# Kernel tuning notes

Hardware: AMD Instinct MI355X
Metric: run time of the kernel (lower is better)

## Reference

```python
import jax, jax.numpy as jnp
import numpy as np


def setup_inputs() -> dict:
    key = jax.random.key(0)
    B, N, D = 8, 2048, 512
    put = jax.random.normal(key, (B, N, D), dtype=jnp.float32)
    return {"put": put, "k": 16}


def reference(put, k):
    # put: [B, N, D]; k: python int
    B, N, _ = put.shape
    # squared-norm expansion of pairwise Euclidean distance
    xx = jnp.sum(put * put, axis=2, keepdims=True)            # [B, N, 1]
    gram = jnp.einsum('bnd,bmd->bnm', put, put)               # [B, N, N]
    dist2 = xx + jnp.swapaxes(xx, 1, 2) - 2.0 * gram          # [B, N, N]
    dist = jnp.sqrt(jnp.clip(dist2, 0.0))                     # clamp(min=0).sqrt()

    # k nearest (smallest distance): top_k of negated distances
    _, inc = jax.lax.top_k(-dist, k)                          # [B, N, k] int32

    # binary adjacency: out[b, j, inc[b, j, :]] = 1 (vectorized scatter)
    b_idx = jnp.arange(B)[:, None, None]                      # [B,1,1]
    r_idx = jnp.arange(N)[None, :, None]                      # [1,N,1]
    out = jnp.zeros_like(dist).at[b_idx, r_idx, inc].set(1.0)
    return out
```

## Files before the change

### kernel.cpp

```cpp
#include <hip/hip_runtime.h>
#include <cstdint>

#define NN 2048
#define DD 512
#define NB 8
#define NCAND 24

using ull = unsigned long long;
typedef __attribute__((ext_vector_type(8))) short bf16x8;
typedef __attribute__((ext_vector_type(4))) float f32x4;

#define GLOAD_LDS16(g, l)                                                      \
  __builtin_amdgcn_global_load_lds(                                            \
      (const __attribute__((address_space(1))) unsigned int*)(g),              \
      (__attribute__((address_space(3))) unsigned int*)(l), 16, 0, 0)

__device__ inline unsigned short f2bf(float f) {
  unsigned u = __float_as_uint(f);
  unsigned r = u + 0x7FFFu + ((u >> 16) & 1u);
  return (unsigned short)(r >> 16);
}

__global__ __launch_bounds__(256) void knn_prep(const float* __restrict__ put,
                                                float* __restrict__ norms32,
                                                unsigned short* __restrict__ bhalf) {
  const int row  = blockIdx.x * 4 + (threadIdx.x >> 6);
  const int lane = threadIdx.x & 63;
  const float* p = put + (size_t)row * DD + lane * 8;
  float4 x0 = ((const float4*)p)[0];
  float4 x1 = ((const float4*)p)[1];
  double s = (double)x0.x * (double)x0.x + (double)x0.y * (double)x0.y +
             (double)x0.z * (double)x0.z + (double)x0.w * (double)x0.w +
             (double)x1.x * (double)x1.x + (double)x1.y * (double)x1.y +
             (double)x1.z * (double)x1.z + (double)x1.w * (double)x1.w;
  uint4 v;
  v.x = (unsigned)f2bf(x0.x) | ((unsigned)f2bf(x0.y) << 16);
  v.y = (unsigned)f2bf(x0.z) | ((unsigned)f2bf(x0.w) << 16);
  v.z = (unsigned)f2bf(x1.x) | ((unsigned)f2bf(x1.y) << 16);
  v.w = (unsigned)f2bf(x1.z) | ((unsigned)f2bf(x1.w) << 16);
  *((uint4*)(bhalf + (size_t)row * DD) + lane) = v;
#pragma unroll
  for (int m = 1; m < 64; m <<= 1) s += __shfl_xor(s, m, 64);
  if (lane == 0) norms32[row] = (float)s;
}

__global__ __launch_bounds__(256) void knn_gemm(
    const unsigned short* __restrict__ bhalf,
    const float* __restrict__ norms32,
    unsigned short* __restrict__ Sws) {
  __shared__ unsigned short smem[18432];
  unsigned short* As = smem;
  unsigned short* Bs = smem + 4096;

  int idx = blockIdx.x;
  int jt = 0;
  while (idx >= 16 - jt) { idx -= 16 - jt; ++jt; }
  const int mt = jt + idx;

  const int t    = threadIdx.x;
  const int lane = t & 63;
  const int wv   = t >> 6;
  const int q    = lane >> 4;
  const int l15  = lane & 15;
  const int wrow = wv >> 1, wcol = wv & 1;
  const int m0 = mt * 128;
  const int j0 = jt * 128;
  const int b  = blockIdx.y;

  const unsigned short* pb = bhalf + (size_t)b * NN * DD;

  const int rloc = lane >> 2;
  const int kcg  = (lane & 3) ^ ((lane >> 3) & 3);
  const int i0 = 2 * wv, i1 = 2 * wv + 1;
  const unsigned short* gA0 = pb + (size_t)(j0 + 16 * i0 + rloc) * DD + kcg * 8;
  const unsigned short* gA1 = pb + (size_t)(j0 + 16 * i1 + rloc) * DD + kcg * 8;
  const unsigned short* gB0 = pb + (size_t)(m0 + 16 * i0 + rloc) * DD + kcg * 8;
  const unsigned short* gB1 = pb + (size_t)(m0 + 16 * i1 + rloc) * DD + kcg * 8;
  unsigned short* lA0 = As + i0 * 512;
  unsigned short* lA1 = As + i1 * 512;
  unsigned short* lB0 = Bs + i0 * 512;
  unsigned short* lB1 = Bs + i1 * 512;

  const int xsw = (q ^ ((l15 >> 1) & 3)) * 8;

  f32x4 acc[4][4];
  const f32x4 zz = {0.f, 0.f, 0.f, 0.f};
#pragma unroll
  for (int i = 0; i < 4; ++i)
#pragma unroll
    for (int j = 0; j < 4; ++j) acc[i][j] = zz;

  for (int kt = 0; kt < DD; kt += 32) {
    __syncthreads();
    GLOAD_LDS16(gA0, lA0);
    GLOAD_LDS16(gA1, lA1);
    GLOAD_LDS16(gB0, lB0);
    GLOAD_LDS16(gB1, lB1);
    gA0 += 32; gA1 += 32; gB0 += 32; gB1 += 32;
    __syncthreads();

    bf16x8 af[4], bg[4];
#pragma unroll
    for (int f = 0; f < 4; ++f) {
      af[f] = *(const bf16x8*)(As + (wrow * 64 + f * 16 + l15) * 32 + xsw);
      bg[f] = *(const bf16x8*)(Bs + (wcol * 64 + f * 16 + l15) * 32 + xsw);
    }
#pragma unroll
    for (int fi = 0; fi < 4; ++fi)
#pragma unroll
      for (int fj = 0; fj < 4; ++fj)
        acc[fi][fj] = __builtin_amdgcn_mfma_f32_16x16x32_bf16(
            af[fi], bg[fj], acc[fi][fj], 0, 0, 0);
  }

  float xn[4];
#pragma unroll
  for (int fj = 0; fj < 4; ++fj)
    xn[fj] = norms32[(size_t)b * NN + m0 + wcol * 64 + fj * 16 + l15];

  __syncthreads();
  unsigned short* Sl = smem + wv * 4096;
#pragma unroll
  for (int fi = 0; fi < 4; ++fi)
#pragma unroll
    for (int fj = 0; fj < 4; ++fj)
#pragma unroll
      for (int r = 0; r < 4; ++r) {
        float sv = xn[fj] - 2.0f * acc[fi][fj][r] + 2048.0f;
        Sl[(fi * 16 + q * 4 + r) * 64 + fj * 16 + l15] =
            __builtin_bit_cast(unsigned short, (_Float16)sv);
      }

  const size_t row0 = (size_t)(b * NN + j0 + wrow * 64);
#pragma unroll
  for (int it = 0; it < 8; ++it) {
    int i2 = it * 64 + lane;
    int row = i2 >> 3, c8 = i2 & 7;
    uint4 v = *(const uint4*)(Sl + row * 64 + c8 * 8);
    *(uint4*)(Sws + (row0 + row) * NN + m0 + wcol * 64 + c8 * 8) = v;
  }

  if (jt != mt) {
    float xr[16];
#pragma unroll
    for (int fi = 0; fi < 4; ++fi)
#pragma unroll
      for (int r = 0; r < 4; ++r)
        xr[fi * 4 + r] =
            norms32[(size_t)b * NN + j0 + wrow * 64 + fi * 16 + q * 4 + r];

    __syncthreads();
    unsigned short* Mw = smem + wv * 4608;
#pragma unroll
    for (int fi = 0; fi < 4; ++fi)
#pragma unroll
      for (int fj = 0; fj < 4; ++fj)
#pragma unroll
        for (int r = 0; r < 4; ++r) {
          float sv = xr[fi * 4 + r] - 2.0f * acc[fi][fj][r] + 2048.0f;
          Mw[(fj * 16 + l15) * 72 + fi * 16 + q * 4 + r] =
              __builtin_bit_cast(unsigned short, (_Float16)sv);
        }
    const size_t mrow0 = (size_t)(b * NN + m0 + wcol * 64);
#pragma unroll
    for (int it = 0; it < 8; ++it) {
      int i2 = it * 64 + lane;
      int row = i2 >> 3, c8 = i2 & 7;
      uint4 v = *(const uint4*)(Mw + row * 72 + c8 * 8);
      *(uint4*)(Sws + (mrow0 + row) * NN + j0 + wrow * 64 + c8 * 8) = v;
    }
  }
}

#define CEX(a, i, j)                                                           \
  {                                                                            \
    unsigned lo_ = min(a[i], a[j]), hi_ = max(a[i], a[j]);                     \
    a[i] = lo_;                                                                \
    a[j] = hi_;                                                                \
  }

__device__ inline void mk8(unsigned (&a)[8], uint4 u, unsigned base) {
  a[0] = (u.x << 16) | base;
  a[1] = (u.x & 0xFFFF0000u) | (base + 1);
  a[2] = (u.y << 16) | (base + 2);
  a[3] = (u.y & 0xFFFF0000u) | (base + 3);
  a[4] = (u.z << 16) | (base + 4);
  a[5] = (u.z & 0xFFFF0000u) | (base + 5);
  a[6] = (u.w << 16) | (base + 6);
  a[7] = (u.w & 0xFFFF0000u) | (base + 7);
}

__device__ inline void sort8(unsigned (&a)[8]) {
  CEX(a, 0, 1) CEX(a, 2, 3) CEX(a, 4, 5) CEX(a, 6, 7)
  CEX(a, 0, 2) CEX(a, 1, 3) CEX(a, 4, 6) CEX(a, 5, 7)
  CEX(a, 1, 2) CEX(a, 5, 6)
  CEX(a, 0, 4) CEX(a, 1, 5) CEX(a, 2, 6) CEX(a, 3, 7)
  CEX(a, 2, 4) CEX(a, 3, 5)
  CEX(a, 1, 2) CEX(a, 3, 4) CEX(a, 5, 6)
}

__device__ inline void merge8(unsigned (&a)[8], const unsigned (&b)[8]) {
  unsigned t[8];
#pragma unroll
  for (int i = 0; i < 8; ++i) t[i] = min(a[i], b[7 - i]);
  CEX(t, 0, 4) CEX(t, 1, 5) CEX(t, 2, 6) CEX(t, 3, 7)
  CEX(t, 0, 2) CEX(t, 1, 3) CEX(t, 4, 6) CEX(t, 5, 7)
  CEX(t, 0, 1) CEX(t, 2, 3) CEX(t, 4, 5) CEX(t, 6, 7)
#pragma unroll
  for (int i = 0; i < 8; ++i) a[i] = t[i];
}

__global__ __launch_bounds__(256) void knn_select(
    const unsigned short* __restrict__ Sws,
    const float* __restrict__ put,
    const float* __restrict__ norms32,
    float* __restrict__ out) {
  __shared__ unsigned candL[4][NCAND];
  __shared__ double part[4][NCAND][9];
  __shared__ ull keyL[4][NCAND];
  __shared__ unsigned winL[4][16];

  const int wv   = threadIdx.x >> 6;
  const int lane = threadIdx.x & 63;
  const int R = blockIdx.x * 4 + wv;
  const int b = R >> 11, j = R & (NN - 1);

  const unsigned short* Srow = Sws + (size_t)R * NN;
  uint4 u0 = *(const uint4*)(Srow + 0 * 512 + lane * 8);
  uint4 u1 = *(const uint4*)(Srow + 1 * 512 + lane * 8);
  uint4 u2 = *(const uint4*)(Srow + 2 * 512 + lane * 8);
  uint4 u3 = *(const uint4*)(Srow + 3 * 512 + lane * 8);
  unsigned h[8], c1[8], c2[8], c3[8];
  mk8(h, u0, (unsigned)(0 * 512 + lane * 8));
  mk8(c1, u1, (unsigned)(1 * 512 + lane * 8));
  mk8(c2, u2, (unsigned)(2 * 512 + lane * 8));
  mk8(c3, u3, (unsigned)(3 * 512 + lane * 8));
  sort8(h); sort8(c1); sort8(c2); sort8(c3);
  merge8(h, c1);
  merge8(c2, c3);
  merge8(h, c2);

#pragma unroll
  for (int pass = 0; pass < NCAND / 2; ++pass) {
    unsigned a1 = h[0], a2 = h[1];
#pragma unroll
    for (int m = 1; m < 64; m <<= 1) {
      unsigned b1 = (unsigned)__shfl_xor((int)a1, m, 64);
      unsigned b2 = (unsigned)__shfl_xor((int)a2, m, 64);
      unsigned lo  = min(a1, b1);
      unsigned mid = max(a1, b1);
      unsigned hi  = min(a2, b2);
      a1 = lo;
      a2 = min(mid, hi);
    }
    if ((h[0] == a1) | (h[0] == a2)) {
#pragma unroll
      for (int p = 0; p < 7; ++p) h[p] = h[p + 1];
      h[7] = 0xFFFFFFFFu;
    }
    if (h[0] == a2) {
#pragma unroll
      for (int p = 0; p < 7; ++p) h[p] = h[p + 1];
      h[7] = 0xFFFFFFFFu;
    }
    if (lane == 0) {
      candL[wv][2 * pass]     = a1 & 0xFFFFu;
      candL[wv][2 * pass + 1] = a2 & 0xFFFFu;
    }
  }

  const float* panel = put + (size_t)b * NN * DD;
  const float* xjp = panel + (size_t)j * DD + lane * 8;
  float4 xa = ((const float4*)xjp)[0];
  float4 xb = ((const float4*)xjp)[1];
  double x0 = xa.x, x1 = xa.y, x2 = xa.z, x3 = xa.w;
  double x4 = xb.x, x5 = xb.y, x6 = xb.z, x7 = xb.w;

  for (int c0 = 0; c0 < NCAND; c0 += 4) {
    double p[4];
#pragma unroll
    for (int uu = 0; uu < 4; ++uu) {
      int cand = __builtin_amdgcn_readfirstlane((int)candL[wv][c0 + uu]);
      const float4* cr = (const float4*)(panel + (size_t)cand * DD + lane * 8);
      float4 ya = cr[0];
      float4 yb = cr[1];
      p[uu] = x0 * (double)ya.x + x1 * (double)ya.y + x2 * (double)ya.z +
              x3 * (double)ya.w + x4 * (double)yb.x + x5 * (double)yb.y +
              x6 * (double)yb.z + x7 * (double)yb.w;
    }
#pragma unroll
    for (int uu = 0; uu < 4; ++uu) {
      p[uu] += __shfl_xor(p[uu], 1, 64);
      p[uu] += __shfl_xor(p[uu], 2, 64);
      p[uu] += __shfl_xor(p[uu], 4, 64);
      if ((lane & 7) == 0) part[wv][c0 + uu][lane >> 3] = p[uu];
    }
  }

  if (lane < NCAND) {
    double dot = part[wv][lane][0] + part[wv][lane][1] + part[wv][lane][2] +
                 part[wv][lane][3] + part[wv][lane][4] + part[wv][lane][5] +
                 part[wv][lane][6] + part[wv][lane][7];
    int cand = (int)candL[wv][lane];
    float g32 = (float)dot;
    float xxm = norms32[(size_t)b * NN + cand];
    float xxj = norms32[(size_t)b * NN + j];
    float s   = __fadd_rn(xxj, xxm);
    float d2  = __fsub_rn(s, __fmul_rn(2.0f, g32));
    d2 = fmaxf(d2, 0.0f);
    float dist = __fsqrt_rn(d2);
    keyL[wv][lane] = ((ull)__float_as_uint(dist) << 32) | (unsigned)cand;
  }
  if (lane < NCAND) {
    ull mine = keyL[wv][lane];
    int rank = 0;
#pragma unroll
    for (int i = 0; i < NCAND; ++i) rank += (keyL[wv][i] < mine) ? 1 : 0;
    if (rank < 16) winL[wv][rank] = (unsigned)(keyL[wv][lane] & 0xFFFFULL);
  }

  unsigned mask = 0;
#pragma unroll
  for (int i = 0; i < 16; ++i) {
    unsigned c = winL[wv][i];
    unsigned own = (((c >> 2) & 63u) == (unsigned)lane) ? 1u : 0u;
    unsigned bit = (((c >> 8) & 7u) << 2) | (c & 3u);
    mask |= own << bit;
  }
  float* orow = out + (size_t)R * NN;
#pragma unroll
  for (int it = 0; it < 8; ++it) {
    float4 v;
    v.x = (float)((mask >> (it * 4 + 0)) & 1u);
    v.y = (float)((mask >> (it * 4 + 1)) & 1u);
    v.z = (float)((mask >> (it * 4 + 2)) & 1u);
    v.w = (float)((mask >> (it * 4 + 3)) & 1u);
    ((float4*)(orow + it * 256))[lane] = v;
  }
}

extern "C" void kernel_launch(void* const* d_in, const int* in_sizes, int n_in,
                              void* d_out, int out_size, void* d_ws, size_t ws_size,
                              hipStream_t stream) {
  const float* put = (const float*)d_in[0];
  float* out = (float*)d_out;

  float* norms32 = (float*)d_ws;
  unsigned short* bhalf = (unsigned short*)((char*)d_ws + 65536);
  unsigned short* Sws =
      (unsigned short*)((char*)d_ws + 65536 + (size_t)NB * NN * DD * 2);

  knn_prep<<<dim3(NB * NN / 4), 256, 0, stream>>>(put, norms32, bhalf);
  knn_gemm<<<dim3(136, NB), 256, 0, stream>>>(bhalf, norms32, Sws);
  knn_select<<<dim3(NB * NN / 4), 256, 0, stream>>>(Sws, put, norms32, out);
}
```

Baseline: 248.5 us.

## Fuse per-tile top-12 selection into GEMM epilogue, drop full fp16 score matrix

The GEMM epilogue now stages each 128x128 fp16 score tile in shared memory, and pairs of threads run a bitonic top-16 selection per row, writing 12 candidate keys per row per tile. Previously the full N×N fp16 distance matrix was written out. The select kernel then reads 192 keys per row instead of 2048 halfs and keeps only 3 registers per lane instead of 8 sorted keys. This removes most of the large intermediate write and read traffic. In exchange it adds sorting work and register pressure to the GEMM epilogue, which also sets a launch-bounds occupancy hint of 3 blocks.

```diff
diff --git a/kernel.cpp b/kernel.cpp
--- a/kernel.cpp
+++ b/kernel.cpp
@@ -19,6 +19,92 @@
   unsigned u = __float_as_uint(f);
   unsigned r = u + 0x7FFFu + ((u >> 16) & 1u);
   return (unsigned short)(r >> 16);
+}
+
+#define CEX(a, i, j)                                                           \
+  {                                                                            \
+    unsigned lo_ = min(a[i], a[j]), hi_ = max(a[i], a[j]);                     \
+    a[i] = lo_;                                                                \
+    a[j] = hi_;                                                                \
+  }
+
+__device__ __forceinline__ void sort8(unsigned (&a)[8]) {
+  CEX(a, 0, 1) CEX(a, 2, 3) CEX(a, 4, 5) CEX(a, 6, 7)
+  CEX(a, 0, 2) CEX(a, 1, 3) CEX(a, 4, 6) CEX(a, 5, 7)
+  CEX(a, 1, 2) CEX(a, 5, 6)
+  CEX(a, 0, 4) CEX(a, 1, 5) CEX(a, 2, 6) CEX(a, 3, 7)
+  CEX(a, 2, 4) CEX(a, 3, 5)
+  CEX(a, 1, 2) CEX(a, 3, 4) CEX(a, 5, 6)
+}
+
+__device__ __forceinline__ void clean16(unsigned (&r)[16]) {
+#pragma unroll
+  for (int d = 8; d >= 1; d >>= 1) {
+#pragma unroll
+    for (int i = 0; i < 16; ++i)
+      if ((i & d) == 0) CEX(r, i, i + d)
+  }
+}
+
+__device__ __forceinline__ void merge16_full(const unsigned (&a)[8],
+                                             const unsigned (&b)[8],
+                                             unsigned (&r)[16]) {
+#pragma unroll
+  for (int i = 0; i < 8; ++i) { r[i] = a[i]; r[15 - i] = b[i]; }
+  clean16(r);
+}
+
+__device__ __forceinline__ void top16(unsigned (&a)[16], const unsigned (&b)[16]) {
+  unsigned t[16];
+#pragma unroll
+  for (int i = 0; i < 16; ++i) t[i] = min(a[i], b[15 - i]);
+  clean16(t);
+#pragma unroll
+  for (int i = 0; i < 16; ++i) a[i] = t[i];
+}
+
+__device__ __forceinline__ void load8(unsigned (&a)[8], const unsigned short* p,
+                                      unsigned c0) {
+  uint4 u = *(const uint4*)p;
+  a[0] = (u.x << 16) | c0;
+  a[1] = (u.x & 0xFFFF0000u) | (c0 + 1);
+  a[2] = (u.y << 16) | (c0 + 2);
+  a[3] = (u.y & 0xFFFF0000u) | (c0 + 3);
+  a[4] = (u.z << 16) | (c0 + 4);
+  a[5] = (u.z & 0xFFFF0000u) | (c0 + 5);
+  a[6] = (u.w << 16) | (c0 + 6);
+  a[7] = (u.w & 0xFFFF0000u) | (c0 + 7);
+}
+
+__device__ __forceinline__ void sel_write(const unsigned short* S,
+                                          unsigned* __restrict__ Kws, int b,
+                                          int rowbase, int tile, int colbase,
+                                          int t) {
+  const int row = t >> 1, half = t & 1;
+  const unsigned short* Sr = S + row * 136 + half * 64;
+  const unsigned cb = (unsigned)(colbase + half * 64);
+  unsigned m[16], s0[8], s1[8], n16[16];
+  load8(s0, Sr + 0, cb + 0);
+  load8(s1, Sr + 8, cb + 8);
+  sort8(s0); sort8(s1);
+  merge16_full(s0, s1, m);
+#pragma unroll
+  for (int c = 16; c < 64; c += 16) {
+    load8(s0, Sr + c, cb + c);
+    load8(s1, Sr + c + 8, cb + c + 8);
+    sort8(s0); sort8(s1);
+    merge16_full(s0, s1, n16);
+    top16(m, n16);
+  }
+  unsigned o[16];
+#pragma unroll
+  for (int i = 0; i < 16; ++i) o[i] = (unsigned)__shfl_xor((int)m[i], 1, 64);
+  top16(m, o);
+  if (half == 0) {
+    unsigned* dst = Kws + ((size_t)(b * NN + rowbase + row) * 16 + tile) * 12;
+#pragma unroll
+    for (int i = 0; i < 12; ++i) dst[i] = m[i];
+  }
 }
 
 __global__ __launch_bounds__(256) void knn_prep(const float* __restrict__ put,
@@ -44,11 +130,11 @@
   if (lane == 0) norms32[row] = (float)s;
 }
 
-__global__ __launch_bounds__(256) void knn_gemm(
+__global__ __launch_bounds__(256, 3) void knn_gemm(
     const unsigned short* __restrict__ bhalf,
     const float* __restrict__ norms32,
-    unsigned short* __restrict__ Sws) {
-  __shared__ unsigned short smem[18432];
+    unsigned* __restrict__ Kws) {
+  __shared__ unsigned short smem[17408];
   unsigned short* As = smem;
   unsigned short* Bs = smem + 4096;
 
@@ -119,7 +205,6 @@
     xn[fj] = norms32[(size_t)b * NN + m0 + wcol * 64 + fj * 16 + l15];
 
   __syncthreads();
-  unsigned short* Sl = smem + wv * 4096;
 #pragma unroll
   for (int fi = 0; fi < 4; ++fi)
 #pragma unroll
@@ -127,18 +212,11 @@
 #pragma unroll
       for (int r = 0; r < 4; ++r) {
         float sv = xn[fj] - 2.0f * acc[fi][fj][r] + 2048.0f;
-        Sl[(fi * 16 + q * 4 + r) * 64 + fj * 16 + l15] =
+        smem[(wrow * 64 + fi * 16 + q * 4 + r) * 136 + wcol * 64 + fj * 16 + l15] =
             __builtin_bit_cast(unsigned short, (_Float16)sv);
       }
-
-  const size_t row0 = (size_t)(b * NN + j0 + wrow * 64);
-#pragma unroll
-  for (int it = 0; it < 8; ++it) {
-    int i2 = it * 64 + lane;
-    int row = i2 >> 3, c8 = i2 & 7;
-    uint4 v = *(const uint4*)(Sl + row * 64 + c8 * 8);
-    *(uint4*)(Sws + (row0 + row) * NN + m0 + wcol * 64 + c8 * 8) = v;
-  }
+  __syncthreads();
+  sel_write(smem, Kws, b, j0, mt, m0, t);
 
   if (jt != mt) {
     float xr[16];
@@ -150,7 +228,6 @@
             norms32[(size_t)b * NN + j0 + wrow * 64 + fi * 16 + q * 4 + r];
 
     __syncthreads();
-    unsigned short* Mw = smem + wv * 4608;
 #pragma unroll
     for (int fi = 0; fi < 4; ++fi)
 #pragma unroll
@@ -158,60 +235,16 @@
 #pragma unroll
         for (int r = 0; r < 4; ++r) {
           float sv = xr[fi * 4 + r] - 2.0f * acc[fi][fj][r] + 2048.0f;
-          Mw[(fj * 16 + l15) * 72 + fi * 16 + q * 4 + r] =
+          smem[(wcol * 64 + fj * 16 + l15) * 136 + wrow * 64 + fi * 16 + q * 4 + r] =
               __builtin_bit_cast(unsigned short, (_Float16)sv);
         }
-    const size_t mrow0 = (size_t)(b * NN + m0 + wcol * 64);
-#pragma unroll
-    for (int it = 0; it < 8; ++it) {
-      int i2 = it * 64 + lane;
-      int row = i2 >> 3, c8 = i2 & 7;
-      uint4 v = *(const uint4*)(Mw + row * 72 + c8 * 8);
-      *(uint4*)(Sws + (mrow0 + row) * NN + j0 + wrow * 64 + c8 * 8) = v;
-    }
-  }
-}
-
-#define CEX(a, i, j)                                                           \
-  {                                                                            \
-    unsigned lo_ = min(a[i], a[j]), hi_ = max(a[i], a[j]);                     \
-    a[i] = lo_;                                                                \
-    a[j] = hi_;                                                                \
-  }
-
-__device__ inline void mk8(unsigned (&a)[8], uint4 u, unsigned base) {
-  a[0] = (u.x << 16) | base;
-  a[1] = (u.x & 0xFFFF0000u) | (base + 1);
-  a[2] = (u.y << 16) | (base + 2);
-  a[3] = (u.y & 0xFFFF0000u) | (base + 3);
-  a[4] = (u.z << 16) | (base + 4);
-  a[5] = (u.z & 0xFFFF0000u) | (base + 5);
-  a[6] = (u.w << 16) | (base + 6);
-  a[7] = (u.w & 0xFFFF0000u) | (base + 7);
-}
-
-__device__ inline void sort8(unsigned (&a)[8]) {
-  CEX(a, 0, 1) CEX(a, 2, 3) CEX(a, 4, 5) CEX(a, 6, 7)
-  CEX(a, 0, 2) CEX(a, 1, 3) CEX(a, 4, 6) CEX(a, 5, 7)
-  CEX(a, 1, 2) CEX(a, 5, 6)
-  CEX(a, 0, 4) CEX(a, 1, 5) CEX(a, 2, 6) CEX(a, 3, 7)
-  CEX(a, 2, 4) CEX(a, 3, 5)
-  CEX(a, 1, 2) CEX(a, 3, 4) CEX(a, 5, 6)
-}
-
-__device__ inline void merge8(unsigned (&a)[8], const unsigned (&b)[8]) {
-  unsigned t[8];
-#pragma unroll
-  for (int i = 0; i < 8; ++i) t[i] = min(a[i], b[7 - i]);
-  CEX(t, 0, 4) CEX(t, 1, 5) CEX(t, 2, 6) CEX(t, 3, 7)
-  CEX(t, 0, 2) CEX(t, 1, 3) CEX(t, 4, 6) CEX(t, 5, 7)
-  CEX(t, 0, 1) CEX(t, 2, 3) CEX(t, 4, 5) CEX(t, 6, 7)
-#pragma unroll
-  for (int i = 0; i < 8; ++i) a[i] = t[i];
+    __syncthreads();
+    sel_write(smem, Kws, b, m0, jt, j0, t);
+  }
 }
 
 __global__ __launch_bounds__(256) void knn_select(
-    const unsigned short* __restrict__ Sws,
+    const unsigned* __restrict__ Kws,
     const float* __restrict__ put,
     const float* __restrict__ norms32,
     float* __restrict__ out) {
@@ -225,20 +258,9 @@
   const int R = blockIdx.x * 4 + wv;
   const int b = R >> 11, j = R & (NN - 1);
 
-  const unsigned short* Srow = Sws + (size_t)R * NN;
-  uint4 u0 = *(const uint4*)(Srow + 0 * 512 + lane * 8);
-  uint4 u1 = *(const uint4*)(Srow + 1 * 512 + lane * 8);
-  uint4 u2 = *(const uint4*)(Srow + 2 * 512 + lane * 8);
-  uint4 u3 = *(const uint4*)(Srow + 3 * 512 + lane * 8);
-  unsigned h[8], c1[8], c2[8], c3[8];
-  mk8(h, u0, (unsigned)(0 * 512 + lane * 8));
-  mk8(c1, u1, (unsigned)(1 * 512 + lane * 8));
-  mk8(c2, u2, (unsigned)(2 * 512 + lane * 8));
-  mk8(c3, u3, (unsigned)(3 * 512 + lane * 8));
-  sort8(h); sort8(c1); sort8(c2); sort8(c3);
-  merge8(h, c1);
-  merge8(c2, c3);
-  merge8(h, c2);
+  const unsigned* Krow = Kws + (size_t)R * 192 + lane * 3;
+  unsigned h[3] = {Krow[0], Krow[1], Krow[2]};
+  CEX(h, 0, 1) CEX(h, 1, 2) CEX(h, 0, 1)
 
 #pragma unroll
   for (int pass = 0; pass < NCAND / 2; ++pass) {
@@ -253,16 +275,8 @@
       a1 = lo;
       a2 = min(mid, hi);
     }
-    if ((h[0] == a1) | (h[0] == a2)) {
-#pragma unroll
-      for (int p = 0; p < 7; ++p) h[p] = h[p + 1];
-      h[7] = 0xFFFFFFFFu;
-    }
-    if (h[0] == a2) {
-#pragma unroll
-      for (int p = 0; p < 7; ++p) h[p] = h[p + 1];
-      h[7] = 0xFFFFFFFFu;
-    }
+    if ((h[0] == a1) | (h[0] == a2)) { h[0] = h[1]; h[1] = h[2]; h[2] = 0xFFFFFFFFu; }
+    if (h[0] == a2)                  { h[0] = h[1]; h[1] = h[2]; h[2] = 0xFFFFFFFFu; }
     if (lane == 0) {
       candL[wv][2 * pass]     = a1 & 0xFFFFu;
       candL[wv][2 * pass + 1] = a2 & 0xFFFFu;
@@ -347,10 +361,10 @@
 
   float* norms32 = (float*)d_ws;
   unsigned short* bhalf = (unsigned short*)((char*)d_ws + 65536);
-  unsigned short* Sws =
-      (unsigned short*)((char*)d_ws + 65536 + (size_t)NB * NN * DD * 2);
+  unsigned* Kws =
+      (unsigned*)((char*)d_ws + 65536 + (size_t)NB * NN * DD * 2);
 
   knn_prep<<<dim3(NB * NN / 4), 256, 0, stream>>>(put, norms32, bhalf);
-  knn_gemm<<<dim3(136, NB), 256, 0, stream>>>(bhalf, norms32, Sws);
-  knn_select<<<dim3(NB * NN / 4), 256, 0, stream>>>(Sws, put, norms32, out);
-}
+  knn_gemm<<<dim3(136, NB), 256, 0, stream>>>(bhalf, norms32, Kws);
+  knn_select<<<dim3(NB * NN / 4), 256, 0, stream>>>(Kws, put, norms32, out);
+}
```

Result: no change. 249.4 us (+0.4%).
